# Performance work log

Hardware: AMD Instinct MI355X
Metric: run time of the kernel (lower is better)

Reference implementation:

```python
import jax, jax.numpy as jnp
import numpy as np

N_QUBITS = 11
N_CIRCUITS = 3
N_ROTS = 6
BATCH = 512
C64 = jnp.complex64


def _ry_mat(theta):
    # RY(t) = [[cos t/2, -sin t/2], [sin t/2, cos t/2]]
    c = jnp.cos(theta * 0.5)
    s = jnp.sin(theta * 0.5)
    return jnp.stack([jnp.stack([c, -s]), jnp.stack([s, c])]).astype(C64)


def _rz_mat(theta):
    # RZ(t) = diag(e^{-i t/2}, e^{+i t/2})
    e = jnp.exp((-0.5j) * theta.astype(C64))
    z = jnp.zeros_like(e)
    return jnp.stack([jnp.stack([e, z]), jnp.stack([z, jnp.conj(e)])])


def _apply_1q(state, U, q):
    # state: (2,)*n complex; apply 2x2 U on axis q (PennyLane wire q = axis q)
    out = jnp.tensordot(U, state, axes=((1,), (q,)))
    return jnp.moveaxis(out, 0, q)


def _apply_ctrl(state, U, c, t):
    # controlled-U on wires [c(control), t(target)]: block_diag(I2, U) in |c t> basis
    U4 = jnp.eye(4, dtype=C64).at[2:, 2:].set(U)
    out = jnp.tensordot(U4.reshape(2, 2, 2, 2), state, axes=((2, 3), (c, t)))
    return jnp.moveaxis(out, (0, 1), (c, t))


def _simulate(angles):
    # angles: [n_circuits, 6, n_qubits] -> expvals [2*n_qubits] (X then Z)
    n = N_QUBITS
    state = jnp.zeros((2,) * n, dtype=C64).at[(0,) * n].set(1.0)
    for i in range(N_CIRCUITS):
        for q in range(n):
            state = _apply_1q(state, _ry_mat(angles[i, 0, q]), q)
            state = _apply_1q(state, _rz_mat(angles[i, 1, q]), q)
            state = _apply_1q(state, _ry_mat(angles[i, 2, q]), q)
            state = _apply_1q(state, _rz_mat(angles[i, 3, q]), q)
        for q in range(n):
            t = (q + 1) % n
            state = _apply_ctrl(state, _ry_mat(angles[i, 4, q]), q, t)
            state = _apply_ctrl(state, _rz_mat(angles[i, 5, q]), q, t)
    ex_x, ex_z = [], []
    for q in range(n):
        s0 = jnp.take(state, 0, axis=q)
        s1 = jnp.take(state, 1, axis=q)
        # <X_q> = 2 Re <psi_{q=0}|psi_{q=1}>,  <Z_q> = p(q=0) - p(q=1)
        ex_x.append(2.0 * jnp.real(jnp.vdot(s0, s1)))
        ex_z.append(jnp.sum(jnp.abs(s0) ** 2 - jnp.abs(s1) ** 2))
    return jnp.stack(ex_x + ex_z).astype(jnp.float32)


def setup_inputs() -> dict:
    key = jax.random.key(0)
    k1, k2, k3 = jax.random.split(key, 3)
    x = jax.random.normal(k1, (BATCH, N_QUBITS), dtype=jnp.float32)
    W = jax.random.uniform(k2, (N_CIRCUITS, N_QUBITS * N_ROTS, N_QUBITS),
                           dtype=jnp.float32, minval=-0.01, maxval=0.01)
    b = jax.random.uniform(k3, (N_CIRCUITS, N_QUBITS * N_ROTS),
                           dtype=jnp.float32, minval=-0.01, maxval=0.01)
    return {"x": x, "W": W, "b": b}


def reference(x, W, b):
    # per-circuit Linear (dropout is identity in eval): [B, C, n_rots*n_qubits]
    rot = jnp.einsum('coi,bi->bco', W, x) + b[None, :, :]
    angles = rot.reshape(x.shape[0], N_CIRCUITS, N_ROTS, N_QUBITS)
    return jax.vmap(_simulate)(angles)  # [B, 2*n_qubits]
```

## Files before the change

### kernel.cpp

```cpp
#include <hip/hip_runtime.h>

#define NQ 11
#define NC 3
#define NANG (NC * 66)
#define BLOCK 512

typedef float f2 __attribute__((ext_vector_type(2)));

__device__ __forceinline__ f2 swp(f2 v) { return __builtin_shufflevector(v, v, 1, 0); }

template<int CTRL>
__device__ __forceinline__ float dppx(float v) {
  return __int_as_float(__builtin_amdgcn_update_dpp(
      0, __float_as_int(v), CTRL, 0xF, 0xF, false));
}
template<int CTRL>
__device__ __forceinline__ f2 dpp2(f2 v) {
  f2 r; r.x = dppx<CTRL>(v.x); r.y = dppx<CTRL>(v.y); return r;
}
template<int OFF>
__device__ __forceinline__ float swz1(float v) {
  return __int_as_float(__builtin_amdgcn_ds_swizzle(__float_as_int(v), OFF));
}
template<int OFF>
__device__ __forceinline__ f2 swz2(f2 v) {
  f2 r; r.x = swz1<OFF>(v.x); r.y = swz1<OFF>(v.y); return r;
}
__device__ __forceinline__ float plp16(float v, int lane) {
  auto r = __builtin_amdgcn_permlane16_swap(__float_as_int(v), __float_as_int(v), false, false);
  return __int_as_float((lane & 16) ? r[0] : r[1]);
}
__device__ __forceinline__ float plp32(float v, int lane) {
  auto r = __builtin_amdgcn_permlane32_swap(__float_as_int(v), __float_as_int(v), false, false);
  return __int_as_float((lane & 32) ? r[0] : r[1]);
}
__device__ __forceinline__ f2 plp16_2(f2 v, int lane) {
  f2 r; r.x = plp16(v.x, lane); r.y = plp16(v.y, lane); return r;
}
__device__ __forceinline__ f2 plp32_2(f2 v, int lane) {
  f2 r; r.x = plp32(v.x, lane); r.y = plp32(v.y, lane); return r;
}
__device__ __forceinline__ float plsum16(float v) {
  auto r = __builtin_amdgcn_permlane16_swap(__float_as_int(v), __float_as_int(v), false, false);
  return __int_as_float(r[0]) + __int_as_float(r[1]);
}
__device__ __forceinline__ float plsum32(float v) {
  auto r = __builtin_amdgcn_permlane32_swap(__float_as_int(v), __float_as_int(v), false, false);
  return __int_as_float(r[0]) + __int_as_float(r[1]);
}

__device__ __forceinline__ void apply2p(f2& v0, f2& v1, float4 U) {
  const f2 ai2 = {-U.y, U.y};
  const f2 bi2 = {-U.w, U.w};
  const f2 w0 = swp(v0), w1 = swp(v1);
  const f2 n0 =  U.x * v0 + ai2 * w0 + U.z * v1 + bi2 * w1;
  const f2 n1 = -U.z * v0 + bi2 * w0 + U.x * v1 - ai2 * w1;
  v0 = n0; v1 = n1;
}
__device__ __forceinline__ void gpartp(f2& v, f2 p, float4 U, bool hi) {
  const f2 ai2 = hi ? f2{U.y, -U.y} : f2{-U.y, U.y};
  const float br = hi ? -U.z : U.z;
  const f2 bi2 = {-U.w, U.w};
  v = U.x * v + ai2 * swp(v) + br * p + bi2 * swp(p);
}

template<int OFF, int M>
__device__ __forceinline__ void g_swz(f2 (&s)[4], float4 U, int lane) {
  const bool hi = (lane & M) != 0;
#pragma unroll
  for (int i = 0; i < 4; ++i) gpartp(s[i], swz2<OFF>(s[i]), U, hi);
}
template<int CTRL, int M>
__device__ __forceinline__ void g_dpp(f2 (&s)[4], float4 U, int lane) {
  const bool hi = (lane & M) != 0;
#pragma unroll
  for (int i = 0; i < 4; ++i) gpartp(s[i], dpp2<CTRL>(s[i]), U, hi);
}
__device__ __forceinline__ void g_pl16(f2 (&s)[4], float4 U, int lane) {
  const bool hi = (lane & 16) != 0;
#pragma unroll
  for (int i = 0; i < 4; ++i) gpartp(s[i], plp16_2(s[i], lane), U, hi);
}
__device__ __forceinline__ void g_pl32_regsel(f2 (&s)[4], float4 U0, float4 U1, int lane) {
  const bool hi = (lane & 32) != 0;
#pragma unroll
  for (int i = 0; i < 4; ++i)
    gpartp(s[i], plp32_2(s[i], lane), (i & 1) ? U1 : U0, hi);
}
template<int WVX>
__device__ __forceinline__ void g_wave(f2 (&s)[4], float4 U, f2* buf, int wave, int lane) {
  const int base = (wave << 6) | lane;
#pragma unroll
  for (int i = 0; i < 4; ++i) buf[(i << 9) | base] = s[i];
  __syncthreads();
  const int pbase = ((wave ^ WVX) << 6) | lane;
  const bool hi = (wave & WVX) != 0;
#pragma unroll
  for (int i = 0; i < 4; ++i) gpartp(s[i], buf[(i << 9) | pbase], U, hi);
}

__global__ __launch_bounds__(BLOCK) void qsim_kernel(
    const float* __restrict__ x, const float* __restrict__ W,
    const float* __restrict__ bias, float* __restrict__ out) {
  const int bidx = blockIdx.x;
  const int tid = threadIdx.x;
  const int lane = tid & 63, wave = tid >> 6;

  __shared__ float xs[NQ];
  __shared__ float ang[NANG];
  __shared__ float4 m1s[NC * NQ];
  __shared__ float4 m2s[NC * NQ];
  __shared__ float4 v1s[NC * 10];
  __shared__ f2 ex0[2048];
  __shared__ f2 ex1[2048];
  __shared__ float red[8][24];

  if (tid < NQ) xs[tid] = x[bidx * NQ + tid];
  __syncthreads();

  if (tid < NANG) {
    const int c = tid / 66, o = tid - c * 66;
    const float* wr = W + (c * 66 + o) * NQ;
    float s = bias[c * 66 + o];
#pragma unroll
    for (int i = 0; i < NQ; ++i) s += wr[i] * xs[i];
    ang[tid] = s;
  }
  __syncthreads();

  if (tid < 2 * NC * NQ) {
    const int kind = tid / (NC * NQ);
    const int id = tid - kind * (NC * NQ);
    const int c = id / NQ, q = id - c * NQ;
    const float* a = ang + c * 66;
    if (kind == 0) {
      float s0,c0,s1,c1,s2,c2,s3,c3;
      sincosf(0.5f*a[q],      &s0,&c0);
      sincosf(0.5f*a[11+q],   &s1,&c1);
      sincosf(0.5f*a[22+q],   &s2,&c2);
      sincosf(0.5f*a[33+q],   &s3,&c3);
      const float mar = c1*c0, mai = -s1*c0;
      const float mbr = -c1*s0, mbi = s1*s0;
      const float nar = c2*mar + s2*mbr, nai = c2*mai - s2*mbi;
      const float nbr = c2*mbr - s2*mar, nbi = c2*mbi + s2*mai;
      m1s[id] = make_float4(c3*nar + s3*nai, c3*nai - s3*nar,
                            c3*nbr + s3*nbi, c3*nbi - s3*nbr);
    } else {
      float s4,c4,s5,c5;
      sincosf(0.5f*a[44+q], &s4,&c4);
      sincosf(0.5f*a[55+q], &s5,&c5);
      m2s[id] = make_float4(c5*c4, -s5*c4, -c5*s4, s5*s4);
    }
  }
  __syncthreads();

  if (tid < NC * 10) {
    const int c = tid / 10, tt = tid - c * 10, t = tt + 1;
    const float4 A = m2s[c*NQ + t - 1];
    const float4 B = m1s[c*NQ + t];
    const float pr_=A.x, pi_=A.y, qr_=A.z, qi_=A.w;
    const float ar_=B.x, ai_=B.y, br_=B.z, bi_=B.w;
    v1s[c*10 + tt] = make_float4(
      (pr_*ar_ - pi_*ai_) - (qr_*br_ + qi_*bi_),
      (pr_*ai_ + pi_*ar_) - (qi_*br_ - qr_*bi_),
      (pr_*br_ - pi_*bi_) + (qr_*ar_ + qi_*ai_),
      (pr_*bi_ + pi_*br_) + (qi_*ar_ - qr_*ai_));
  }
  __syncthreads();

  f2 s[4];
#pragma unroll
  for (int i = 0; i < 4; ++i) s[i] = f2{0.f, 0.f};
  if (tid == 0) s[0].x = 1.f;

  int par = 0;
#pragma unroll
  for (int c = 0; c < NC; ++c) {
    const float4* M1 = &m1s[c * NQ];
    const float4* VF = &v1s[c * 10];
    const float4 u0  = M1[0];
    const float4 u1a = M1[1];
    const float4 u1b = VF[0];
    const float4 u2  = *((lane & 32) ? &VF[1] : &M1[2]);
    const float4 u3  = *((lane & 16) ? &VF[2] : &M1[3]);
    const float4 u4  = *((lane & 8)  ? &VF[3] : &M1[4]);
    const float4 u5  = *((wave & 4)  ? &VF[4] : &M1[5]);
    const float4 u6  = *((wave & 2)  ? &VF[5] : &M1[6]);
    const float4 u7  = *((wave & 1)  ? &VF[6] : &M1[7]);
    const float4 u8  = *((lane & 4)  ? &VF[7] : &M1[8]);
    const float4 u9  = *((lane & 2)  ? &VF[8] : &M1[9]);
    const float4 u10 = *((lane & 1)  ? &VF[9] : &M1[10]);
    const float4 u11 = m2s[c * NQ + 10];

    {
      apply2p(s[0], s[1], u0);
      apply2p(s[2], s[3], u0);
    }
    g_pl32_regsel(s, u1a, u1b, lane);
    g_pl16(s, u2, lane);
    g_swz<0x201F,8>(s, u3, lane);
    g_wave<4>(s, u4, par ? ex1 : ex0, wave, lane); par ^= 1;
    g_wave<2>(s, u5, par ? ex1 : ex0, wave, lane); par ^= 1;
    g_wave<1>(s, u6, par ? ex1 : ex0, wave, lane); par ^= 1;
    g_swz<0x101F,4>(s, u7, lane);
    g_dpp<0x4E,2>(s, u8, lane);
    g_dpp<0xB1,1>(s, u9, lane);
    {
      apply2p(s[0], s[2], u10);
      apply2p(s[1], s[3], u10);
    }
    {
      apply2p(s[2], s[3], u11);
    }
  }

  f2* eb = par ? ex1 : ex0;
  const int base = (wave << 6) | lane;
#pragma unroll
  for (int i = 0; i < 4; ++i) eb[(i << 9) | base] = s[i];
  __syncthreads();
  const int pb4 = ((wave ^ 4) << 6) | lane;
  const int pb2 = ((wave ^ 2) << 6) | lane;
  const int pb1 = ((wave ^ 1) << 6) | lane;
  f2 aq4 = {0,0}, aq5 = {0,0}, aq6 = {0,0};
#pragma unroll
  for (int i = 0; i < 4; ++i) {
    aq4 += s[i] * eb[(i << 9) | pb4];
    aq5 += s[i] * eb[(i << 9) | pb2];
    aq6 += s[i] * eb[(i << 9) | pb1];
  }
  f2 mg[4];
#pragma unroll
  for (int i = 0; i < 4; ++i) mg[i] = s[i] * s[i];
  const f2 ztv  = (mg[0] + mg[1]) + (mg[2] + mg[3]);
  const f2 z0v  = (mg[0] - mg[1]) + (mg[2] - mg[3]);
  const f2 z10v = (mg[0] + mg[1]) - (mg[2] + mg[3]);
  f2 aq0={0,0}, aq10={0,0}, aq9={0,0}, aq8={0,0}, aq7={0,0}, aq3={0,0}, aq2={0,0}, aq1={0,0};
#pragma unroll
  for (int i = 0; i < 4; ++i) {
    aq0  += s[i] * s[i ^ 1];
    aq10 += s[i] * s[i ^ 2];
    aq9  += s[i] * dpp2<0xB1>(s[i]);
    aq8  += s[i] * dpp2<0x4E>(s[i]);
    aq7  += s[i] * swz2<0x101F>(s[i]);
    aq3  += s[i] * swz2<0x201F>(s[i]);
    aq2  += s[i] * plp16_2(s[i], lane);
    aq1  += s[i] * plp32_2(s[i], lane);
  }
  const float ztot = ztv.x + ztv.y;

  float v[22];
  v[0]=aq0.x+aq0.y; v[1]=aq1.x+aq1.y; v[2]=aq2.x+aq2.y; v[3]=aq3.x+aq3.y;
  v[4]=aq4.x+aq4.y; v[5]=aq5.x+aq5.y; v[6]=aq6.x+aq6.y;
  v[7]=aq7.x+aq7.y; v[8]=aq8.x+aq8.y; v[9]=aq9.x+aq9.y; v[10]=aq10.x+aq10.y;
  v[11] = z0v.x + z0v.y;
  v[12] = (lane & 32) ? -ztot : ztot;
  v[13] = (lane & 16) ? -ztot : ztot;
  v[14] = (lane & 8)  ? -ztot : ztot;
  v[15] = (wave & 4)  ? -ztot : ztot;
  v[16] = (wave & 2)  ? -ztot : ztot;
  v[17] = (wave & 1)  ? -ztot : ztot;
  v[18] = (lane & 4)  ? -ztot : ztot;
  v[19] = (lane & 2)  ? -ztot : ztot;
  v[20] = (lane & 1)  ? -ztot : ztot;
  v[21] = z10v.x + z10v.y;

#pragma unroll
  for (int k = 0; k < 22; ++k) {
    v[k] += dppx<0xB1>(v[k]);
    v[k] += dppx<0x4E>(v[k]);
  }
  const int q4l = lane & 3;
  float wv[6];
#pragma unroll
  for (int p = 0; p < 5; ++p)
    wv[p] = q4l == 0 ? v[4*p] : (q4l == 1 ? v[4*p+1] : (q4l == 2 ? v[4*p+2] : v[4*p+3]));
  wv[5] = q4l == 0 ? v[20] : (q4l == 1 ? v[21] : 0.f);
#pragma unroll
  for (int p = 0; p < 6; ++p) {
    wv[p] += swz1<0x101F>(wv[p]);
    wv[p] += swz1<0x201F>(wv[p]);
    wv[p] = plsum16(wv[p]);
    wv[p] = plsum32(wv[p]);
  }
  if (lane < 4) {
#pragma unroll
    for (int p = 0; p < 6; ++p) red[wave][4*p + lane] = wv[p];
  }
  __syncthreads();
  if (tid < 22) {
    float sacc = 0.f;
#pragma unroll
    for (int w8 = 0; w8 < 8; ++w8) sacc += red[w8][tid];
    out[bidx * 22 + tid] = sacc;
  }
}

extern "C" void kernel_launch(void* const* d_in, const int* in_sizes, int n_in,
                              void* d_out, int out_size, void* d_ws, size_t ws_size,
                              hipStream_t stream) {
  (void)n_in; (void)d_ws; (void)ws_size; (void)out_size;
  const float* x = (const float*)d_in[0];
  const float* W = (const float*)d_in[1];
  const float* b = (const float*)d_in[2];
  float* out = (float*)d_out;
  const int batch = in_sizes[0] / NQ;
  qsim_kernel<<<batch, BLOCK, 0, stream>>>(x, W, b, out);
}
```

Measured before the change: 21.35 us.

## Spread statevector over 1024 threads with two amplitudes per thread

Doubles the block to 1024 threads, so each thread holds 2 complex amplitudes instead of 4. One more qubit is mapped to the wave index, which means four shared-memory exchange stages per circuit layer instead of three. The circuit loop is no longer unrolled, and the final reductions are adjusted for 16 waves. This trades fewer registers and more parallelism per batch element for an extra block-wide barrier per layer and larger blocks, which may limit residency.

```diff
diff --git a/kernel.cpp b/kernel.cpp
--- a/kernel.cpp
+++ b/kernel.cpp
@@ -3,7 +3,7 @@
 #define NQ 11
 #define NC 3
 #define NANG (NC * 66)
-#define BLOCK 512
+#define BLOCK 1024
 
 typedef float f2 __attribute__((ext_vector_type(2)));
 
@@ -64,42 +64,19 @@
   v = U.x * v + ai2 * swp(v) + br * p + bi2 * swp(p);
 }
 
-template<int OFF, int M>
-__device__ __forceinline__ void g_swz(f2 (&s)[4], float4 U, int lane) {
-  const bool hi = (lane & M) != 0;
-#pragma unroll
-  for (int i = 0; i < 4; ++i) gpartp(s[i], swz2<OFF>(s[i]), U, hi);
-}
-template<int CTRL, int M>
-__device__ __forceinline__ void g_dpp(f2 (&s)[4], float4 U, int lane) {
-  const bool hi = (lane & M) != 0;
-#pragma unroll
-  for (int i = 0; i < 4; ++i) gpartp(s[i], dpp2<CTRL>(s[i]), U, hi);
-}
-__device__ __forceinline__ void g_pl16(f2 (&s)[4], float4 U, int lane) {
-  const bool hi = (lane & 16) != 0;
-#pragma unroll
-  for (int i = 0; i < 4; ++i) gpartp(s[i], plp16_2(s[i], lane), U, hi);
-}
-__device__ __forceinline__ void g_pl32_regsel(f2 (&s)[4], float4 U0, float4 U1, int lane) {
-  const bool hi = (lane & 32) != 0;
-#pragma unroll
-  for (int i = 0; i < 4; ++i)
-    gpartp(s[i], plp32_2(s[i], lane), (i & 1) ? U1 : U0, hi);
-}
 template<int WVX>
-__device__ __forceinline__ void g_wave(f2 (&s)[4], float4 U, f2* buf, int wave, int lane) {
-  const int base = (wave << 6) | lane;
-#pragma unroll
-  for (int i = 0; i < 4; ++i) buf[(i << 9) | base] = s[i];
-  __syncthreads();
-  const int pbase = ((wave ^ WVX) << 6) | lane;
+__device__ __forceinline__ void g_wave(f2& s0, f2& s1, float4 U,
+                                       f2* __restrict__ buf, int wave, int lane) {
+  const int idx = (wave << 6) | lane;
+  buf[idx] = s0; buf[1024 + idx] = s1;
+  __syncthreads();
+  const int p = ((wave ^ WVX) << 6) | lane;
   const bool hi = (wave & WVX) != 0;
-#pragma unroll
-  for (int i = 0; i < 4; ++i) gpartp(s[i], buf[(i << 9) | pbase], U, hi);
-}
-
-__global__ __launch_bounds__(BLOCK) void qsim_kernel(
+  gpartp(s0, buf[p], U, hi);
+  gpartp(s1, buf[1024 + p], U, hi);
+}
+
+__global__ __launch_bounds__(BLOCK, 8) void qsim_kernel(
     const float* __restrict__ x, const float* __restrict__ W,
     const float* __restrict__ bias, float* __restrict__ out) {
   const int bidx = blockIdx.x;
@@ -113,7 +90,7 @@
   __shared__ float4 v1s[NC * 10];
   __shared__ f2 ex0[2048];
   __shared__ f2 ex1[2048];
-  __shared__ float red[8][24];
+  __shared__ float red[16][24];
 
   if (tid < NQ) xs[tid] = x[bidx * NQ + tid];
   __syncthreads();
@@ -168,102 +145,98 @@
   }
   __syncthreads();
 
-  f2 s[4];
-#pragma unroll
-  for (int i = 0; i < 4; ++i) s[i] = f2{0.f, 0.f};
-  if (tid == 0) s[0].x = 1.f;
-
-  int par = 0;
-#pragma unroll
+  f2 s0 = {0.f, 0.f}, s1 = {0.f, 0.f};
+  if (tid == 0) s0.x = 1.f;
+
   for (int c = 0; c < NC; ++c) {
     const float4* M1 = &m1s[c * NQ];
     const float4* VF = &v1s[c * 10];
-    const float4 u0  = M1[0];
-    const float4 u1a = M1[1];
-    const float4 u1b = VF[0];
-    const float4 u2  = *((lane & 32) ? &VF[1] : &M1[2]);
-    const float4 u3  = *((lane & 16) ? &VF[2] : &M1[3]);
-    const float4 u4  = *((lane & 8)  ? &VF[3] : &M1[4]);
-    const float4 u5  = *((wave & 4)  ? &VF[4] : &M1[5]);
-    const float4 u6  = *((wave & 2)  ? &VF[5] : &M1[6]);
-    const float4 u7  = *((wave & 1)  ? &VF[6] : &M1[7]);
-    const float4 u8  = *((lane & 4)  ? &VF[7] : &M1[8]);
-    const float4 u9  = *((lane & 2)  ? &VF[8] : &M1[9]);
-    const float4 u10 = *((lane & 1)  ? &VF[9] : &M1[10]);
-    const float4 u11 = m2s[c * NQ + 10];
-
-    {
-      apply2p(s[0], s[1], u0);
-      apply2p(s[2], s[3], u0);
-    }
-    g_pl32_regsel(s, u1a, u1b, lane);
-    g_pl16(s, u2, lane);
-    g_swz<0x201F,8>(s, u3, lane);
-    g_wave<4>(s, u4, par ? ex1 : ex0, wave, lane); par ^= 1;
-    g_wave<2>(s, u5, par ? ex1 : ex0, wave, lane); par ^= 1;
-    g_wave<1>(s, u6, par ? ex1 : ex0, wave, lane); par ^= 1;
-    g_swz<0x101F,4>(s, u7, lane);
-    g_dpp<0x4E,2>(s, u8, lane);
-    g_dpp<0xB1,1>(s, u9, lane);
-    {
-      apply2p(s[0], s[2], u10);
-      apply2p(s[1], s[3], u10);
-    }
-    {
-      apply2p(s[2], s[3], u11);
-    }
-  }
-
-  f2* eb = par ? ex1 : ex0;
-  const int base = (wave << 6) | lane;
-#pragma unroll
-  for (int i = 0; i < 4; ++i) eb[(i << 9) | base] = s[i];
-  __syncthreads();
-  const int pb4 = ((wave ^ 4) << 6) | lane;
-  const int pb2 = ((wave ^ 2) << 6) | lane;
-  const int pb1 = ((wave ^ 1) << 6) | lane;
-  f2 aq4 = {0,0}, aq5 = {0,0}, aq6 = {0,0};
-#pragma unroll
-  for (int i = 0; i < 4; ++i) {
-    aq4 += s[i] * eb[(i << 9) | pb4];
-    aq5 += s[i] * eb[(i << 9) | pb2];
-    aq6 += s[i] * eb[(i << 9) | pb1];
-  }
-  f2 mg[4];
-#pragma unroll
-  for (int i = 0; i < 4; ++i) mg[i] = s[i] * s[i];
-  const f2 ztv  = (mg[0] + mg[1]) + (mg[2] + mg[3]);
-  const f2 z0v  = (mg[0] - mg[1]) + (mg[2] - mg[3]);
-  const f2 z10v = (mg[0] + mg[1]) - (mg[2] + mg[3]);
-  f2 aq0={0,0}, aq10={0,0}, aq9={0,0}, aq8={0,0}, aq7={0,0}, aq3={0,0}, aq2={0,0}, aq1={0,0};
-#pragma unroll
-  for (int i = 0; i < 4; ++i) {
-    aq0  += s[i] * s[i ^ 1];
-    aq10 += s[i] * s[i ^ 2];
-    aq9  += s[i] * dpp2<0xB1>(s[i]);
-    aq8  += s[i] * dpp2<0x4E>(s[i]);
-    aq7  += s[i] * swz2<0x101F>(s[i]);
-    aq3  += s[i] * swz2<0x201F>(s[i]);
-    aq2  += s[i] * plp16_2(s[i], lane);
-    aq1  += s[i] * plp32_2(s[i], lane);
-  }
-  const float ztot = ztv.x + ztv.y;
+    apply2p(s0, s1, M1[0]);
+    {
+      const bool hi = (lane & 32) != 0;
+      gpartp(s0, plp32_2(s0, lane), M1[1], hi);
+      gpartp(s1, plp32_2(s1, lane), VF[0], hi);
+    }
+    {
+      const float4 U = *((lane & 32) ? &VF[1] : &M1[2]);
+      const bool hi = (lane & 16) != 0;
+      gpartp(s0, plp16_2(s0, lane), U, hi);
+      gpartp(s1, plp16_2(s1, lane), U, hi);
+    }
+    {
+      const float4 U = *((lane & 16) ? &VF[2] : &M1[3]);
+      const bool hi = (lane & 8) != 0;
+      gpartp(s0, swz2<0x201F>(s0), U, hi);
+      gpartp(s1, swz2<0x201F>(s1), U, hi);
+    }
+    g_wave<8>(s0, s1, *((lane & 8) ? &VF[3] : &M1[4]), ex0, wave, lane);
+    g_wave<4>(s0, s1, *((wave & 8) ? &VF[4] : &M1[5]), ex1, wave, lane);
+    g_wave<2>(s0, s1, *((wave & 4) ? &VF[5] : &M1[6]), ex0, wave, lane);
+    g_wave<1>(s0, s1, *((wave & 2) ? &VF[6] : &M1[7]), ex1, wave, lane);
+    {
+      const float4 U = *((wave & 1) ? &VF[7] : &M1[8]);
+      const bool hi = (lane & 4) != 0;
+      gpartp(s0, swz2<0x101F>(s0), U, hi);
+      gpartp(s1, swz2<0x101F>(s1), U, hi);
+    }
+    {
+      const float4 U = *((lane & 4) ? &VF[8] : &M1[9]);
+      const bool hi = (lane & 2) != 0;
+      gpartp(s0, dpp2<0x4E>(s0), U, hi);
+      gpartp(s1, dpp2<0x4E>(s1), U, hi);
+    }
+    {
+      const float4 U = *((lane & 2) ? &VF[9] : &M1[10]);
+      const bool hi = (lane & 1) != 0;
+      gpartp(s0, dpp2<0xB1>(s0), U, hi);
+      gpartp(s1, dpp2<0xB1>(s1), U, hi);
+    }
+    {
+      const float4 Uc = m2s[c * NQ + 10];
+      const float4 U = (lane & 1) ? Uc : make_float4(1.f, 0.f, 0.f, 0.f);
+      apply2p(s0, s1, U);
+    }
+  }
+
+  const int idx = (wave << 6) | lane;
+  ex0[idx] = s0; ex0[1024 + idx] = s1;
+  __syncthreads();
+  const int p8 = ((wave ^ 8) << 6) | lane;
+  const int p4 = ((wave ^ 4) << 6) | lane;
+  const int p2 = ((wave ^ 2) << 6) | lane;
+  const int p1 = ((wave ^ 1) << 6) | lane;
+  f2 t;
+  t = s0*ex0[p8] + s1*ex0[1024+p8]; const float xq4 = t.x + t.y;
+  t = s0*ex0[p4] + s1*ex0[1024+p4]; const float xq5 = t.x + t.y;
+  t = s0*ex0[p2] + s1*ex0[1024+p2]; const float xq6 = t.x + t.y;
+  t = s0*ex0[p1] + s1*ex0[1024+p1]; const float xq7 = t.x + t.y;
+
+  const f2 mg0 = s0 * s0, mg1 = s1 * s1;
+  const float m0 = mg0.x + mg0.y, m1 = mg1.x + mg1.y;
+  const float ztot = m0 + m1;
+  const float zq0 = m0 - m1;
+  t = s0 * s1; const float xq0 = 2.f * (t.x + t.y);
+  t = s0*plp32_2(s0,lane) + s1*plp32_2(s1,lane); const float xq1 = t.x + t.y;
+  t = s0*plp16_2(s0,lane) + s1*plp16_2(s1,lane); const float xq2 = t.x + t.y;
+  t = s0*swz2<0x201F>(s0) + s1*swz2<0x201F>(s1); const float xq3 = t.x + t.y;
+  t = s0*swz2<0x101F>(s0) + s1*swz2<0x101F>(s1); const float xq8 = t.x + t.y;
+  t = s0*dpp2<0x4E>(s0)  + s1*dpp2<0x4E>(s1);  const float xq9 = t.x + t.y;
+  t = s0*dpp2<0xB1>(s0)  + s1*dpp2<0xB1>(s1);  const float xq10 = t.x + t.y;
 
   float v[22];
-  v[0]=aq0.x+aq0.y; v[1]=aq1.x+aq1.y; v[2]=aq2.x+aq2.y; v[3]=aq3.x+aq3.y;
-  v[4]=aq4.x+aq4.y; v[5]=aq5.x+aq5.y; v[6]=aq6.x+aq6.y;
-  v[7]=aq7.x+aq7.y; v[8]=aq8.x+aq8.y; v[9]=aq9.x+aq9.y; v[10]=aq10.x+aq10.y;
-  v[11] = z0v.x + z0v.y;
+  v[0]=xq0; v[1]=xq1; v[2]=xq2; v[3]=xq3; v[4]=xq4; v[5]=xq5; v[6]=xq6;
+  v[7]=xq7; v[8]=xq8; v[9]=xq9; v[10]=xq10;
+  v[11] = zq0;
   v[12] = (lane & 32) ? -ztot : ztot;
   v[13] = (lane & 16) ? -ztot : ztot;
   v[14] = (lane & 8)  ? -ztot : ztot;
-  v[15] = (wave & 4)  ? -ztot : ztot;
-  v[16] = (wave & 2)  ? -ztot : ztot;
-  v[17] = (wave & 1)  ? -ztot : ztot;
-  v[18] = (lane & 4)  ? -ztot : ztot;
-  v[19] = (lane & 2)  ? -ztot : ztot;
-  v[20] = (lane & 1)  ? -ztot : ztot;
-  v[21] = z10v.x + z10v.y;
+  v[15] = (wave & 8)  ? -ztot : ztot;
+  v[16] = (wave & 4)  ? -ztot : ztot;
+  v[17] = (wave & 2)  ? -ztot : ztot;
+  v[18] = (wave & 1)  ? -ztot : ztot;
+  v[19] = (lane & 4)  ? -ztot : ztot;
+  v[20] = (lane & 2)  ? -ztot : ztot;
+  v[21] = (lane & 1)  ? -ztot : ztot;
 
 #pragma unroll
   for (int k = 0; k < 22; ++k) {
@@ -291,7 +264,7 @@
   if (tid < 22) {
     float sacc = 0.f;
 #pragma unroll
-    for (int w8 = 0; w8 < 8; ++w8) sacc += red[w8][tid];
+    for (int w16 = 0; w16 < 16; ++w16) sacc += red[w16][tid];
     out[bidx * 22 + tid] = sacc;
   }
 }
```

Result: slower. 24.27 us (+13.7%).

## Fuse three cross-wave qubit gates into one 8x8 exchange with a single barrier

Applied to the files above, without the earlier changes.

The three consecutive gates on the qubits held in the wave-index bits become one combined 8x8 operator. Each thread builds its row from the tensor product of the three 2x2 rows and gathers all eight partner amplitudes from shared memory after a single barrier. This drops two __syncthreads and two store/load rounds per circuit layer. The cost is eight LDS reads and more complex multiply-adds per amplitude instead of one. The circuit loop is also no longer unrolled, buffer parity is keyed on the layer index, and gate matrices are loaded from shared memory at their point of use.

```diff
diff --git a/kernel.cpp b/kernel.cpp
--- a/kernel.cpp
+++ b/kernel.cpp
@@ -64,39 +64,39 @@
   v = U.x * v + ai2 * swp(v) + br * p + bi2 * swp(p);
 }
 
-template<int OFF, int M>
-__device__ __forceinline__ void g_swz(f2 (&s)[4], float4 U, int lane) {
-  const bool hi = (lane & M) != 0;
-#pragma unroll
-  for (int i = 0; i < 4; ++i) gpartp(s[i], swz2<OFF>(s[i]), U, hi);
-}
-template<int CTRL, int M>
-__device__ __forceinline__ void g_dpp(f2 (&s)[4], float4 U, int lane) {
-  const bool hi = (lane & M) != 0;
-#pragma unroll
-  for (int i = 0; i < 4; ++i) gpartp(s[i], dpp2<CTRL>(s[i]), U, hi);
-}
-__device__ __forceinline__ void g_pl16(f2 (&s)[4], float4 U, int lane) {
-  const bool hi = (lane & 16) != 0;
-#pragma unroll
-  for (int i = 0; i < 4; ++i) gpartp(s[i], plp16_2(s[i], lane), U, hi);
-}
-__device__ __forceinline__ void g_pl32_regsel(f2 (&s)[4], float4 U0, float4 U1, int lane) {
-  const bool hi = (lane & 32) != 0;
-#pragma unroll
-  for (int i = 0; i < 4; ++i)
-    gpartp(s[i], plp32_2(s[i], lane), (i & 1) ? U1 : U0, hi);
-}
-template<int WVX>
-__device__ __forceinline__ void g_wave(f2 (&s)[4], float4 U, f2* buf, int wave, int lane) {
+__device__ __forceinline__ f2 cmul(f2 u, f2 v) {
+  return f2{u.x * v.x - u.y * v.y, u.x * v.y + u.y * v.x};
+}
+__device__ __forceinline__ void rowof(float4 G, bool hi, f2& c0, f2& c1) {
+  c0 = hi ? f2{-G.z, G.w} : f2{G.x, G.y};
+  c1 = hi ? f2{G.x, -G.y} : f2{G.z, G.w};
+}
+
+__device__ __forceinline__ void g_wave3(f2 (&s)[4], float4 A, float4 B, float4 C,
+                                        f2* __restrict__ buf, int wave, int lane) {
   const int base = (wave << 6) | lane;
 #pragma unroll
   for (int i = 0; i < 4; ++i) buf[(i << 9) | base] = s[i];
-  __syncthreads();
-  const int pbase = ((wave ^ WVX) << 6) | lane;
-  const bool hi = (wave & WVX) != 0;
-#pragma unroll
-  for (int i = 0; i < 4; ++i) gpartp(s[i], buf[(i << 9) | pbase], U, hi);
+  f2 a0, a1, b0, b1, c0, c1;
+  rowof(A, (wave & 4) != 0, a0, a1);
+  rowof(B, (wave & 2) != 0, b0, b1);
+  rowof(C, (wave & 1) != 0, c0, c1);
+  const f2 d00 = cmul(b0, c0), d01 = cmul(b0, c1);
+  const f2 d10 = cmul(b1, c0), d11 = cmul(b1, c1);
+  f2 r[8];
+  r[0] = cmul(a0, d00); r[1] = cmul(a0, d01); r[2] = cmul(a0, d10); r[3] = cmul(a0, d11);
+  r[4] = cmul(a1, d00); r[5] = cmul(a1, d01); r[6] = cmul(a1, d10); r[7] = cmul(a1, d11);
+  __syncthreads();
+#pragma unroll
+  for (int i = 0; i < 4; ++i) {
+    f2 acc = {0.f, 0.f};
+#pragma unroll
+    for (int w2 = 0; w2 < 8; ++w2) {
+      const f2 p = buf[(i << 9) | (w2 << 6) | lane];
+      acc += r[w2].x * p + f2{-r[w2].y, r[w2].y} * swp(p);
+    }
+    s[i] = acc;
+  }
 }
 
 __global__ __launch_bounds__(BLOCK) void qsim_kernel(
@@ -173,48 +173,67 @@
   for (int i = 0; i < 4; ++i) s[i] = f2{0.f, 0.f};
   if (tid == 0) s[0].x = 1.f;
 
-  int par = 0;
-#pragma unroll
   for (int c = 0; c < NC; ++c) {
     const float4* M1 = &m1s[c * NQ];
     const float4* VF = &v1s[c * 10];
-    const float4 u0  = M1[0];
-    const float4 u1a = M1[1];
-    const float4 u1b = VF[0];
-    const float4 u2  = *((lane & 32) ? &VF[1] : &M1[2]);
-    const float4 u3  = *((lane & 16) ? &VF[2] : &M1[3]);
-    const float4 u4  = *((lane & 8)  ? &VF[3] : &M1[4]);
-    const float4 u5  = *((wave & 4)  ? &VF[4] : &M1[5]);
-    const float4 u6  = *((wave & 2)  ? &VF[5] : &M1[6]);
-    const float4 u7  = *((wave & 1)  ? &VF[6] : &M1[7]);
-    const float4 u8  = *((lane & 4)  ? &VF[7] : &M1[8]);
-    const float4 u9  = *((lane & 2)  ? &VF[8] : &M1[9]);
-    const float4 u10 = *((lane & 1)  ? &VF[9] : &M1[10]);
-    const float4 u11 = m2s[c * NQ + 10];
-
-    {
-      apply2p(s[0], s[1], u0);
-      apply2p(s[2], s[3], u0);
-    }
-    g_pl32_regsel(s, u1a, u1b, lane);
-    g_pl16(s, u2, lane);
-    g_swz<0x201F,8>(s, u3, lane);
-    g_wave<4>(s, u4, par ? ex1 : ex0, wave, lane); par ^= 1;
-    g_wave<2>(s, u5, par ? ex1 : ex0, wave, lane); par ^= 1;
-    g_wave<1>(s, u6, par ? ex1 : ex0, wave, lane); par ^= 1;
-    g_swz<0x101F,4>(s, u7, lane);
-    g_dpp<0x4E,2>(s, u8, lane);
-    g_dpp<0xB1,1>(s, u9, lane);
-    {
-      apply2p(s[0], s[2], u10);
-      apply2p(s[1], s[3], u10);
-    }
-    {
-      apply2p(s[2], s[3], u11);
-    }
-  }
-
-  f2* eb = par ? ex1 : ex0;
+    {
+      apply2p(s[0], s[1], M1[0]);
+      apply2p(s[2], s[3], M1[0]);
+    }
+    g_pl32_regsel: ;
+    {
+      const bool hi = (lane & 32) != 0;
+#pragma unroll
+      for (int i = 0; i < 4; ++i)
+        gpartp(s[i], plp32_2(s[i], lane), (i & 1) ? VF[0] : M1[1], hi);
+    }
+    {
+      const float4 U = *((lane & 32) ? &VF[1] : &M1[2]);
+      const bool hi = (lane & 16) != 0;
+#pragma unroll
+      for (int i = 0; i < 4; ++i) gpartp(s[i], plp16_2(s[i], lane), U, hi);
+    }
+    {
+      const float4 U = *((lane & 16) ? &VF[2] : &M1[3]);
+      const bool hi = (lane & 8) != 0;
+#pragma unroll
+      for (int i = 0; i < 4; ++i) gpartp(s[i], swz2<0x201F>(s[i]), U, hi);
+    }
+    {
+      const float4 A = *((lane & 8) ? &VF[3] : &M1[4]);
+      const float4 B = *((wave & 4) ? &VF[4] : &M1[5]);
+      const float4 C = *((wave & 2) ? &VF[5] : &M1[6]);
+      g_wave3(s, A, B, C, (c & 1) ? ex1 : ex0, wave, lane);
+    }
+    {
+      const float4 U = *((wave & 1) ? &VF[6] : &M1[7]);
+      const bool hi = (lane & 4) != 0;
+#pragma unroll
+      for (int i = 0; i < 4; ++i) gpartp(s[i], swz2<0x101F>(s[i]), U, hi);
+    }
+    {
+      const float4 U = *((lane & 4) ? &VF[7] : &M1[8]);
+      const bool hi = (lane & 2) != 0;
+#pragma unroll
+      for (int i = 0; i < 4; ++i) gpartp(s[i], dpp2<0x4E>(s[i]), U, hi);
+    }
+    {
+      const float4 U = *((lane & 2) ? &VF[8] : &M1[9]);
+      const bool hi = (lane & 1) != 0;
+#pragma unroll
+      for (int i = 0; i < 4; ++i) gpartp(s[i], dpp2<0xB1>(s[i]), U, hi);
+    }
+    {
+      const float4 U = *((lane & 1) ? &VF[9] : &M1[10]);
+      apply2p(s[0], s[2], U);
+      apply2p(s[1], s[3], U);
+    }
+    {
+      apply2p(s[2], s[3], m2s[c * NQ + 10]);
+    }
+  }
+
+  f2* eb = ex1;
   const int base = (wave << 6) | lane;
 #pragma unroll
   for (int i = 0; i < 4; ++i) eb[(i << 9) | base] = s[i];
```

After: 23.76 us. 1.11x slower.
